# Kernel optimization log

Hardware: AMD Instinct MI355X
Metric: run time of the kernel (lower is better)

Reference implementation:

```python
import jax
import jax.numpy as jnp
from jax import lax
import numpy as np

B, C, H, W = 16, 96, 112, 112
HIDDEN = 4 * C
LN_EPS = 1e-6  # ConvNeXt LayerNorm eps


def setup_inputs() -> dict:
    key = jax.random.key(0)
    ks = jax.random.split(key, 8)
    x = jax.random.normal(ks[0], (B, C, H, W), dtype=jnp.float32)
    # depthwise 7x7 kernel, HWIO with feature_group_count=C -> (7,7,1,C)
    dw_w = jax.random.normal(ks[1], (7, 7, 1, C), dtype=jnp.float32) * 0.02
    dw_b = jnp.zeros((C,), dtype=jnp.float32)
    gamma = jnp.ones((C,), dtype=jnp.float32)
    beta = jnp.zeros((C,), dtype=jnp.float32)
    w1 = jax.random.normal(ks[2], (C, HIDDEN), dtype=jnp.float32) * 0.02
    b1 = jnp.zeros((HIDDEN,), dtype=jnp.float32)
    w2 = jax.random.normal(ks[3], (HIDDEN, C), dtype=jnp.float32) * 0.02
    b2 = jnp.zeros((C,), dtype=jnp.float32)
    scale = jnp.full((C,), 1e-6, dtype=jnp.float32)  # block_scale init 1e-6
    return {"x": x, "dw_w": dw_w, "dw_b": dw_b, "gamma": gamma, "beta": beta,
            "w1": w1, "b1": b1, "w2": w2, "b2": b2, "scale": scale}


def reference(x, dw_w, dw_b, gamma, beta, w1, b1, w2, b2, scale):
    # depthwise 7x7, stride 1, padding 3 (SAME), groups = C
    y = lax.conv_general_dilated(
        x, dw_w, window_strides=(1, 1), padding="SAME",
        dimension_numbers=("NCHW", "HWIO", "NCHW"),
        feature_group_count=C,
    ) + dw_b[None, :, None, None]
    # BCHW -> BHWC
    y = jnp.transpose(y, (0, 2, 3, 1))
    # LayerNorm over channel dim
    mu = jnp.mean(y, axis=-1, keepdims=True)
    var = jnp.var(y, axis=-1, keepdims=True)
    y = (y - mu) * lax.rsqrt(var + LN_EPS) * gamma + beta
    # pointwise MLP with exact GELU (torch nn.GELU default)
    h = jax.nn.gelu(jnp.einsum("bhwc,cd->bhwd", y, w1) + b1, approximate=False)
    y = jnp.einsum("bhwd,dc->bhwc", h, w2) + b2
    # BHWC -> BCHW, scale, residual (eval mode: stochastic depth = identity)
    y = jnp.transpose(y, (0, 3, 1, 2))
    return scale[None, :, None, None] * y + x
```

## Files before the change

### kernel.cpp

```cpp
#include <hip/hip_runtime.h>
#include <hip/hip_bf16.h>

#define BATCH 16
#define CCH 96
#define HH 112
#define WW 112
#define HID 384
#define NPIX (BATCH * HH * WW)
#define HW (HH * WW)

#define PXB 128
#define ZROWD 50
#define HSLICE 6144
#define ZR_BYTES (PXB * ZROWD * 4)
#define B1_OFF ZR_BYTES
#define SMEM_TOTAL (ZR_BYTES + 1536)

typedef __attribute__((ext_vector_type(8))) short bf16x8;
typedef __attribute__((ext_vector_type(4))) float f32x4;
typedef __attribute__((ext_vector_type(4))) unsigned int uint4v;

typedef const __attribute__((address_space(1))) void gvoid_t;
typedef __attribute__((address_space(3))) void svoid_t;

__device__ __forceinline__ short f2bf(float v) {
    __hip_bfloat16 h = __float2bfloat16(v);
    return __builtin_bit_cast(short, h);
}
__device__ __forceinline__ float bf2f(short s) {
    unsigned int u = ((unsigned int)(unsigned short)s) << 16;
    return __builtin_bit_cast(float, u);
}
__device__ __forceinline__ float gelu_fast(float v) {
    float e = __expf(-1.702f * v);
    return v * __builtin_amdgcn_rcpf(1.0f + e);
}

__global__ __launch_bounds__(256) void pack_w(const float* __restrict__ w1,
                                              const float* __restrict__ w2,
                                              const float* __restrict__ gamma,
                                              const float* __restrict__ scale,
                                              short* __restrict__ wp) {
    int o = blockIdx.x * 256 + threadIdx.x;
    if (o >= 12 * 12 * 64 * 8) return;
    const int j   = o & 7;
    const int l   = (o >> 3) & 63;
    const int g   = o >> 9;
    const int f   = g % 12;
    const int kk2 = g / 12;
    float v;
    if (f < 6) {
        const int kk = f >> 1, mh = f & 1;
        const int c  = kk * 32 + (l >> 4) * 8 + j;
        const int d  = (2 * kk2 + mh) * 16 + (l & 15);
        v = gamma[c] * w1[c * HID + d];
    } else {
        const int nt2 = f - 6;
        const int dd  = kk2 * 32 + ((j >> 2) << 4) + ((l >> 4) << 2) + (j & 3);
        const int n   = nt2 * 16 + (l & 15);
        v = w2[dd * CCH + n] * scale[n];
    }
    wp[o] = f2bf(v);
}

__global__ __launch_bounds__(256) void pack_bias(const float* __restrict__ w1,
                                                 const float* __restrict__ b1,
                                                 const float* __restrict__ beta,
                                                 const float* __restrict__ b2,
                                                 const float* __restrict__ scale,
                                                 float* __restrict__ b1p,
                                                 float* __restrict__ b2p) {
    int t = blockIdx.x * 256 + threadIdx.x;
    if (t < HID) {
        float s = b1[t];
        for (int c = 0; c < CCH; ++c) s += beta[c] * w1[c * HID + t];
        b1p[t] = s;
    } else if (t < HID + CCH) {
        int c = t - HID;
        b2p[c] = scale[c] * b2[c];
    }
}

__global__ __launch_bounds__(256) void conv_kernel(
    const float* __restrict__ x, const float* __restrict__ dww,
    const float* __restrict__ dwb, short* __restrict__ y)
{
    __shared__ float xs[34][120];

    const int t = threadIdx.x;
    const int p = blockIdx.x;
    int o = (p & 7) * 768 + (p >> 3);
    const int ht = o & 3;  o >>= 2;
    const int c  = o % CCH;
    const int b  = o / CCH;
    const int h0 = ht * 28;
    const float* xc = x + (size_t)(b * CCH + c) * HW;

    float vbuf[16];
    #pragma unroll
    for (int k = 0; k < 16; ++k) {
        const int idx = t + 256 * k;
        float v = 0.f;
        if (idx < 34 * 120) {
            const int r   = idx / 120;
            const int col = idx - r * 120;
            const int gh  = h0 - 3 + r;
            const int gw  = col - 3;
            if ((unsigned)gh < HH && (unsigned)gw < WW) v = xc[gh * WW + gw];
        }
        vbuf[k] = v;
    }
    #pragma unroll
    for (int k = 0; k < 16; ++k) {
        const int idx = t + 256 * k;
        if (idx < 34 * 120) ((float*)xs)[idx] = vbuf[k];
    }
    __syncthreads();

    const int col = t & 127;
    const int rg  = t >> 7;
    if (col < WW) {
        const int r0 = rg * 14;
        const float bias = dwb[c];
        float acc[14];
        #pragma unroll
        for (int r = 0; r < 14; ++r) acc[r] = bias;
        #pragma unroll
        for (int kw = 0; kw < 7; ++kw) {
            float cv[20];
            #pragma unroll
            for (int i = 0; i < 20; ++i) cv[i] = xs[r0 + i][col + kw];
            #pragma unroll
            for (int kh = 0; kh < 7; ++kh) {
                const float wt = dww[(kh * 7 + kw) * CCH + c];
                #pragma unroll
                for (int r = 0; r < 14; ++r) acc[r] += cv[r + kh] * wt;
            }
        }
        short* yc = y + (size_t)(b * CCH + c) * HW + (h0 + r0) * WW + col;
        #pragma unroll
        for (int r = 0; r < 14; ++r) yc[r * WW] = f2bf(acc[r]);
    }
}

__global__ __launch_bounds__(256, 4) void mlp_kernel(
    const short* __restrict__ ybuf, const char* __restrict__ wp,
    const float* __restrict__ b1p, const float* __restrict__ b2p,
    const float* __restrict__ x, float* __restrict__ out)
{
    __shared__ __align__(16) char smem[SMEM_TOTAL];
    unsigned int* zr = (unsigned int*)smem;
    float* b1l = (float*)(smem + B1_OFF);

    const int t    = threadIdx.x;
    const int lane = t & 63;
    const int wv   = t >> 6;
    const int l15  = lane & 15;
    const int q    = lane >> 4;
    const int px0  = blockIdx.x * PXB;
    const int b    = px0 / HW;
    const int hw0  = px0 - b * HW;
    const int c0 = (wv < 2) ? 2 * wv : wv + 2;
    const int c1 = (wv < 2) ? 2 * wv + 1 : wv + 2;

    if (t < 192) {
        const int pq = t / 48;
        const int cp = t - pq * 48;
        const unsigned int* Ap = (const unsigned int*)(ybuf +
            (size_t)(b * CCH + 2 * cp) * HW + hw0 + pq * 32);
        const unsigned int* Bp = (const unsigned int*)(ybuf +
            (size_t)(b * CCH + 2 * cp + 1) * HW + hw0 + pq * 32);
        #pragma unroll
        for (int e = 0; e < 4; ++e) {
            const uint4v A  = *reinterpret_cast<const uint4v*>(Ap + e * 4);
            const uint4v Bv = *reinterpret_cast<const uint4v*>(Bp + e * 4);
            #pragma unroll
            for (int k = 0; k < 4; ++k) {
                const int px = pq * 32 + e * 8 + 2 * k;
                zr[px * ZROWD + cp]       = (A[k] & 0xffffu) | (Bv[k] << 16);
                zr[(px + 1) * ZROWD + cp] = (A[k] >> 16) | (Bv[k] & 0xffff0000u);
            }
        }
    } else {
        const int i0 = (t - 192) * 6;
        #pragma unroll
        for (int i2 = 0; i2 < 6; ++i2) b1l[i0 + i2] = b1p[i0 + i2];
    }

    f32x4 acc2[2][6];
    #pragma unroll
    for (int nt2 = 0; nt2 < 6; ++nt2) {
        const int c = nt2 * 16 + l15;
        const float bv = b2p[c];
        #pragma unroll
        for (int m2 = 0; m2 < 2; ++m2) {
            const size_t g = (size_t)(b * CCH + c) * HW + hw0 + wv * 32 + m2 * 16 + q * 4;
            const f32x4 xv = *reinterpret_cast<const f32x4*>(x + g);
            acc2[m2][nt2].x = bv + xv.x;  acc2[m2][nt2].y = bv + xv.y;
            acc2[m2][nt2].z = bv + xv.z;  acc2[m2][nt2].w = bv + xv.w;
        }
    }
    __syncthreads();

    bf16x8 za[2][3];
    #pragma unroll
    for (int nt = 0; nt < 2; ++nt) {
        const int row = wv * 32 + nt * 16 + l15;
        const char* base = smem + row * (ZROWD * 4) + q * 16;
        float s1 = 0.f, s2 = 0.f;
        #pragma unroll
        for (int kk = 0; kk < 3; ++kk) {
            za[nt][kk] = *reinterpret_cast<const bf16x8*>(base + kk * 64);
            #pragma unroll
            for (int j = 0; j < 8; ++j) {
                const float v = bf2f(za[nt][kk][j]);
                s1 += v; s2 += v * v;
            }
        }
        s1 += __shfl_xor(s1, 16, 64);  s2 += __shfl_xor(s2, 16, 64);
        s1 += __shfl_xor(s1, 32, 64);  s2 += __shfl_xor(s2, 32, 64);
        const float mu   = s1 * (1.0f / CCH);
        const float rstd = rsqrtf(s2 * (1.0f / CCH) - mu * mu + 1e-6f);
        #pragma unroll
        for (int kk = 0; kk < 3; ++kk)
            #pragma unroll
            for (int j = 0; j < 8; ++j)
                za[nt][kk][j] = f2bf((bf2f(za[nt][kk][j]) - mu) * rstd);
    }
    __syncthreads();

    asm volatile("s_waitcnt vmcnt(0)" ::: "memory");

    #define STAGE_H(HS, SLOT)                                                       \
        {                                                                           \
            const char* _s = wp + (size_t)(HS) * HSLICE + lane * 16;                \
            char* _d = smem + (SLOT) * HSLICE;                                      \
            __builtin_amdgcn_global_load_lds((gvoid_t*)(_s + c0 * 1024),            \
                                             (svoid_t*)(_d + c0 * 1024), 16, 0, 0); \
            __builtin_amdgcn_global_load_lds((gvoid_t*)(_s + c1 * 1024),            \
                                             (svoid_t*)(_d + c1 * 1024), 16, 0, 0); \
        }
    #define WAITBAR()                                                               \
        {                                                                           \
            asm volatile("s_waitcnt vmcnt(4)" ::: "memory");                        \
            __builtin_amdgcn_s_barrier();                                           \
            __builtin_amdgcn_sched_barrier(0);                                      \
        }

    STAGE_H(0, 0);
    STAGE_H(1, 1);

    #pragma unroll
    for (int kk2 = 0; kk2 < 12; ++kk2) {
        {
            const int hs = (2 * kk2 + 2 > 23) ? 23 : 2 * kk2 + 2;
            STAGE_H(hs, hs & 3);
        }
        WAITBAR();
        const char* wb1 = smem + ((2 * kk2) & 3) * HSLICE + lane * 16;

        f32x4 p0[2], p1[2];
        const f32x4 bva = *reinterpret_cast<const f32x4*>(b1l + 32 * kk2 + q * 4);
        const f32x4 bvb = *reinterpret_cast<const f32x4*>(b1l + 32 * kk2 + 16 + q * 4);
        p0[0] = bva;  p0[1] = bva;
        p1[0] = bvb;  p1[1] = bvb;
        #pragma unroll
        for (int kk = 0; kk < 3; ++kk) {
            const bf16x8 wfa = *reinterpret_cast<const bf16x8*>(wb1 + (kk * 2) * 1024);
            const bf16x8 wfb = *reinterpret_cast<const bf16x8*>(wb1 + (kk * 2 + 1) * 1024);
            p0[0] = __builtin_amdgcn_mfma_f32_16x16x32_bf16(wfa, za[0][kk], p0[0], 0, 0, 0);
            p0[1] = __builtin_amdgcn_mfma_f32_16x16x32_bf16(wfa, za[1][kk], p0[1], 0, 0, 0);
            p1[0] = __builtin_amdgcn_mfma_f32_16x16x32_bf16(wfb, za[0][kk], p1[0], 0, 0, 0);
            p1[1] = __builtin_amdgcn_mfma_f32_16x16x32_bf16(wfb, za[1][kk], p1[1], 0, 0, 0);
        }
        bf16x8 hv[2];
        #pragma unroll
        for (int nt = 0; nt < 2; ++nt)
            #pragma unroll
            for (int i = 0; i < 4; ++i) {
                hv[nt][i]     = f2bf(gelu_fast(p0[nt][i]));
                hv[nt][4 + i] = f2bf(gelu_fast(p1[nt][i]));
            }

        {
            const int hs = (2 * kk2 + 3 > 23) ? 23 : 2 * kk2 + 3;
            STAGE_H(hs, hs & 3);
        }
        WAITBAR();
        const char* wb2 = smem + ((2 * kk2 + 1) & 3) * HSLICE + lane * 16;
        #pragma unroll
        for (int nt2 = 0; nt2 < 6; ++nt2) {
            const bf16x8 bfr = *reinterpret_cast<const bf16x8*>(wb2 + nt2 * 1024);
            acc2[0][nt2] = __builtin_amdgcn_mfma_f32_16x16x32_bf16(hv[0], bfr, acc2[0][nt2], 0, 0, 0);
            acc2[1][nt2] = __builtin_amdgcn_mfma_f32_16x16x32_bf16(hv[1], bfr, acc2[1][nt2], 0, 0, 0);
        }
    }
    #undef STAGE_H
    #undef WAITBAR

    #pragma unroll
    for (int m2 = 0; m2 < 2; ++m2) {
        const int pxl = hw0 + wv * 32 + m2 * 16 + q * 4;
        #pragma unroll
        for (int nt2 = 0; nt2 < 6; ++nt2) {
            const int c = nt2 * 16 + l15;
            const size_t g = (size_t)(b * CCH + c) * HW + pxl;
            *reinterpret_cast<f32x4*>(out + g) = acc2[m2][nt2];
        }
    }
}

extern "C" void kernel_launch(void* const* d_in, const int* in_sizes, int n_in,
                              void* d_out, int out_size, void* d_ws, size_t ws_size,
                              hipStream_t stream) {
    const float* x     = (const float*)d_in[0];
    const float* dww   = (const float*)d_in[1];
    const float* dwb   = (const float*)d_in[2];
    const float* gamma = (const float*)d_in[3];
    const float* beta  = (const float*)d_in[4];
    const float* w1    = (const float*)d_in[5];
    const float* b1    = (const float*)d_in[6];
    const float* w2    = (const float*)d_in[7];
    const float* b2    = (const float*)d_in[8];
    const float* scale = (const float*)d_in[9];
    float* out = (float*)d_out;

    char* ws = (char*)d_ws;
    short* ybuf = (short*)ws;
    const size_t Y_BYTES = (size_t)NPIX * CCH * 2;
    short* wp  = (short*)(ws + Y_BYTES);
    float* b1p = (float*)(ws + Y_BYTES + 24 * HSLICE);
    float* b2p = b1p + HID;

    pack_w<<<(12 * 12 * 64 * 8 + 255) / 256, 256, 0, stream>>>(w1, w2, gamma, scale, wp);
    pack_bias<<<2, 256, 0, stream>>>(w1, b1, beta, b2, scale, b1p, b2p);
    conv_kernel<<<BATCH * CCH * 4, 256, 0, stream>>>(x, dww, dwb, ybuf);
    mlp_kernel<<<NPIX / PXB, 256, 0, stream>>>(ybuf, (const char*)wp, b1p, b2p, x, out);
}
```

Baseline: 121.0 us.

## Deepen MLP weight prefetch ring to six slots and vectorize conv halo loads

The MLP kernel's weight-slice ring buffer goes from 4 to 6 LDS slots and is prefetched 4 slices ahead instead of 2, with the vmcnt wait relaxed to match. The goal is to hide more global-load latency behind the MFMA work. Separately, the depthwise conv tile load now uses float4 global loads into a 128-wide padded row, replacing scalar loads with per-element division and modulo. The larger LDS footprint (B1_OFF moves to 36 KB) may reduce occupancy, and the ring sizing has to stay consistent with the smem usage of the z staging area.

```diff
diff --git a/kernel.cpp b/kernel.cpp
--- a/kernel.cpp
+++ b/kernel.cpp
@@ -12,9 +12,10 @@
 #define PXB 128
 #define ZROWD 50
 #define HSLICE 6144
+#define RING_SLOTS 6
 #define ZR_BYTES (PXB * ZROWD * 4)
-#define B1_OFF ZR_BYTES
-#define SMEM_TOTAL (ZR_BYTES + 1536)
+#define B1_OFF (RING_SLOTS * HSLICE)
+#define SMEM_TOTAL (B1_OFF + 1536)
 
 typedef __attribute__((ext_vector_type(8))) short bf16x8;
 typedef __attribute__((ext_vector_type(4))) float f32x4;
@@ -85,7 +86,7 @@
     const float* __restrict__ x, const float* __restrict__ dww,
     const float* __restrict__ dwb, short* __restrict__ y)
 {
-    __shared__ float xs[34][120];
+    __shared__ float xs[34][128];
 
     const int t = threadIdx.x;
     const int p = blockIdx.x;
@@ -96,24 +97,23 @@
     const int h0 = ht * 28;
     const float* xc = x + (size_t)(b * CCH + c) * HW;
 
-    float vbuf[16];
-    #pragma unroll
-    for (int k = 0; k < 16; ++k) {
+    float4 vbuf[5];
+    #pragma unroll
+    for (int k = 0; k < 5; ++k) {
         const int idx = t + 256 * k;
-        float v = 0.f;
-        if (idx < 34 * 120) {
-            const int r   = idx / 120;
-            const int col = idx - r * 120;
-            const int gh  = h0 - 3 + r;
-            const int gw  = col - 3;
-            if ((unsigned)gh < HH && (unsigned)gw < WW) v = xc[gh * WW + gw];
-        }
+        const int r  = idx >> 5;
+        const int j  = idx & 31;
+        const int gh = h0 - 3 + r;
+        float4 v = make_float4(0.f, 0.f, 0.f, 0.f);
+        if (idx < 1088 && (unsigned)gh < HH && j >= 1 && j <= 28)
+            v = *reinterpret_cast<const float4*>(xc + gh * WW + 4 * j - 4);
         vbuf[k] = v;
     }
     #pragma unroll
-    for (int k = 0; k < 16; ++k) {
+    for (int k = 0; k < 5; ++k) {
         const int idx = t + 256 * k;
-        if (idx < 34 * 120) ((float*)xs)[idx] = vbuf[k];
+        if (idx < 1088)
+            *reinterpret_cast<float4*>(&xs[0][0] + (idx >> 5) * 128 + (idx & 31) * 4) = vbuf[k];
     }
     __syncthreads();
 
@@ -129,7 +129,7 @@
         for (int kw = 0; kw < 7; ++kw) {
             float cv[20];
             #pragma unroll
-            for (int i = 0; i < 20; ++i) cv[i] = xs[r0 + i][col + kw];
+            for (int i = 0; i < 20; ++i) cv[i] = xs[r0 + i][col + kw + 1];
             #pragma unroll
             for (int kh = 0; kh < 7; ++kh) {
                 const float wt = dww[(kh * 7 + kw) * CCH + c];
@@ -242,22 +242,24 @@
         }
     #define WAITBAR()                                                               \
         {                                                                           \
-            asm volatile("s_waitcnt vmcnt(4)" ::: "memory");                        \
+            asm volatile("s_waitcnt vmcnt(8)" ::: "memory");                        \
             __builtin_amdgcn_s_barrier();                                           \
             __builtin_amdgcn_sched_barrier(0);                                      \
         }
 
     STAGE_H(0, 0);
     STAGE_H(1, 1);
+    STAGE_H(2, 2);
+    STAGE_H(3, 3);
 
     #pragma unroll
     for (int kk2 = 0; kk2 < 12; ++kk2) {
         {
-            const int hs = (2 * kk2 + 2 > 23) ? 23 : 2 * kk2 + 2;
-            STAGE_H(hs, hs & 3);
+            const int hs = (2 * kk2 + 4 > 23) ? 23 : 2 * kk2 + 4;
+            STAGE_H(hs, hs % RING_SLOTS);
         }
         WAITBAR();
-        const char* wb1 = smem + ((2 * kk2) & 3) * HSLICE + lane * 16;
+        const char* wb1 = smem + ((2 * kk2) % RING_SLOTS) * HSLICE + lane * 16;
 
         f32x4 p0[2], p1[2];
         const f32x4 bva = *reinterpret_cast<const f32x4*>(b1l + 32 * kk2 + q * 4);
@@ -283,11 +285,11 @@
             }
 
         {
-            const int hs = (2 * kk2 + 3 > 23) ? 23 : 2 * kk2 + 3;
-            STAGE_H(hs, hs & 3);
+            const int hs = (2 * kk2 + 5 > 23) ? 23 : 2 * kk2 + 5;
+            STAGE_H(hs, hs % RING_SLOTS);
         }
         WAITBAR();
-        const char* wb2 = smem + ((2 * kk2 + 1) & 3) * HSLICE + lane * 16;
+        const char* wb2 = smem + ((2 * kk2 + 1) % RING_SLOTS) * HSLICE + lane * 16;
         #pragma unroll
         for (int nt2 = 0; nt2 < 6; ++nt2) {
             const bf16x8 bfr = *reinterpret_cast<const bf16x8*>(wb2 + nt2 * 1024);
```

Result: no change. 121.7 us (+0.6%).
